# Kernel optimization log

Hardware: AMD Instinct MI355X
Metric: run time of the kernel (lower is better)

Reference implementation:

```python
import jax, jax.numpy as jnp
import numpy as np

C = 256
GROUPS = 32
EPS = 1e-6


def setup_inputs() -> dict:
    key = jax.random.key(0)
    ks = jax.random.split(key, 11)
    b, c, h, w, d = 4, C, 16, 16, 16
    s = 0.02
    return {
        "x": jax.random.normal(ks[0], (b, c, h, w, d), jnp.float32),
        "gn_w": jnp.ones((c,), jnp.float32),
        "gn_b": jnp.zeros((c,), jnp.float32),
        "wq": jax.random.normal(ks[1], (c, c), jnp.float32) * s,
        "bq": jnp.zeros((c,), jnp.float32),
        "wk": jax.random.normal(ks[2], (c, c), jnp.float32) * s,
        "bk": jnp.zeros((c,), jnp.float32),
        "wv": jax.random.normal(ks[3], (c, c), jnp.float32) * s,
        "bv": jnp.zeros((c,), jnp.float32),
        "wo": jax.random.normal(ks[4], (c, c), jnp.float32) * s,
        "bo": jnp.zeros((c,), jnp.float32),
    }


def group_norm(x, w, b):
    bsz, c, h, wd, d = x.shape
    xg = x.reshape(bsz, GROUPS, c // GROUPS, h, wd, d)
    mean = xg.mean(axis=(2, 3, 4, 5), keepdims=True)
    var = xg.var(axis=(2, 3, 4, 5), keepdims=True)
    xg = (xg - mean) * jax.lax.rsqrt(var + EPS)
    x = xg.reshape(bsz, c, h, wd, d)
    return x * w[None, :, None, None, None] + b[None, :, None, None, None]


def conv1(x, w, b):
    # 1x1x1 conv == channel-mixing matmul; x: [b,c,h,w,d], w: [out,in]
    return jnp.einsum('oc,bchwd->bohwd', w, x) + b[None, :, None, None, None]


def reference(x, gn_w, gn_b, wq, bq, wk, bk, wv, bv, wo, bo):
    b, c, h, w, d = x.shape
    scale = c ** (-0.5)
    xn = group_norm(x, gn_w, gn_b)
    q = conv1(xn, wq, bq).reshape(b, c, h * w * d)
    k = conv1(xn, wk, bk).reshape(b, c, h * w * d)
    v = conv1(xn, wv, bv).reshape(b, c, h * w * d)
    attn = jnp.einsum('bci,bcj->bij', q, k) * scale  # [b, N, N]
    attn = jax.nn.softmax(attn, axis=2)
    out = jnp.einsum('bij,bcj->bci', attn, v).reshape(b, c, h, w, d)
    out = conv1(out, wo, bo)
    return x + out
```

## Files before the change

kernel.cpp:

```cpp
#include <hip/hip_runtime.h>
#include <hip/hip_bf16.h>

#define BB 4
#define CC 256
#define NN 4096
#define BBNN (BB * NN)
#define NGROUPS 32
#define CPG 8
#define EPSG 1e-6f
#define QKSCL 0.30028063f
#define KSPLIT 4
#define JITERS (NN / KSPLIT / 64)
#define KSTRIDE 272

typedef __bf16 bf16x8 __attribute__((ext_vector_type(8)));
typedef float  f32x4  __attribute__((ext_vector_type(4)));

typedef __attribute__((address_space(1))) const void g_void;
typedef __attribute__((address_space(3))) void l_void;

__device__ __forceinline__ unsigned short f2bf(float f) {
  unsigned u = __builtin_bit_cast(unsigned, f);
  u += 0x7fffu + ((u >> 16) & 1u);
  return (unsigned short)(u >> 16);
}
__device__ __forceinline__ float bf2f(unsigned short s) {
  return __builtin_bit_cast(float, (unsigned)s << 16);
}

__device__ __forceinline__ f32x4 mfma16(bf16x8 a, bf16x8 b, f32x4 c) {
  return __builtin_amdgcn_mfma_f32_16x16x32_bf16(a, b, c, 0, 0, 0);
}
__device__ __forceinline__ f32x4 mfma8(long a, long b, f32x4 c) {
  return __builtin_amdgcn_mfma_f32_16x16x32_fp8_fp8(a, b, c, 0, 0, 0);
}

__device__ __forceinline__ bf16x8 ldfrag(const unsigned short* p) {
  return __builtin_bit_cast(bf16x8, *(const uint4*)p);
}

__global__ __launch_bounds__(256) void pre(const float* __restrict__ wq,
    const float* __restrict__ wk, const float* __restrict__ wv,
    const float* __restrict__ wo, const float* __restrict__ x,
    unsigned short* __restrict__ wbf, float* __restrict__ part) {
  if (blockIdx.x < 256) {
    int mat = blockIdx.x >> 6, blk = blockIdx.x & 63;
    const float* s = mat == 0 ? wq : mat == 1 ? wk : mat == 2 ? wv : wo;
    int i = (blk * 256 + threadIdx.x) * 4;
    float4 v = *(const float4*)&s[i];
    unsigned short* d = wbf + (size_t)mat * CC * CC + i;
    d[0] = f2bf(v.x); d[1] = f2bf(v.y); d[2] = f2bf(v.z); d[3] = f2bf(v.w);
    return;
  }
  int bx = blockIdx.x - 256;
  int pair = bx >> 1, h = bx & 1;
  const float* xp = x + (size_t)pair * (CPG * NN) + (size_t)h * (CPG * NN / 2);
  float s = 0.f, s2 = 0.f;
  for (int i = threadIdx.x; i < CPG * NN / 8; i += 256) {
    float4 v = ((const float4*)xp)[i];
    s += v.x + v.y + v.z + v.w;
    s2 += v.x * v.x + v.y * v.y + v.z * v.z + v.w * v.w;
  }
  for (int o = 32; o; o >>= 1) { s += __shfl_down(s, o); s2 += __shfl_down(s2, o); }
  __shared__ float rs[4], rs2[4];
  int wid = threadIdx.x >> 6, lane = threadIdx.x & 63;
  if (lane == 0) { rs[wid] = s; rs2[wid] = s2; }
  __syncthreads();
  if (threadIdx.x == 0) {
    part[bx * 2 + 0] = rs[0] + rs[1] + rs[2] + rs[3];
    part[bx * 2 + 1] = rs2[0] + rs2[1] + rs2[2] + rs2[3];
  }
}

__global__ __launch_bounds__(256) void gqkv(const float* __restrict__ x,
    const float* __restrict__ gw, const float* __restrict__ gb,
    const float* __restrict__ part, const unsigned short* __restrict__ wbf,
    const float* __restrict__ bq, const float* __restrict__ bk,
    const float* __restrict__ bv,
    unsigned char* __restrict__ q8, unsigned char* __restrict__ k8,
    unsigned char* __restrict__ v8) {
  const int low = blockIdx.x & 7;
  const int b = low & 3, shalf = low >> 2;
  const int t = blockIdx.x >> 3;
  const int mode = t >> 5;
  const int u = t & 31;
  const int sidx = (u >> 4) * 2 + shalf;
  const int nt = sidx * 16 + (u & 15);
  const int n0 = nt * 64;
  __shared__ unsigned short Xs[64][CC + 8];
  int tid = threadIdx.x;
  const float* xb = x + (size_t)b * CC * NN;
#pragma unroll
  for (int tt = 0; tt < 2; ++tt) {
    int item = tt * 256 + tid;
    int g = item >> 4, nc = item & 15;
    int pair = b * NGROUPS + g;
    float s = part[pair * 4 + 0] + part[pair * 4 + 2];
    float s2 = part[pair * 4 + 1] + part[pair * 4 + 3];
    float mean = s / (CPG * NN);
    float inv = rsqrtf(s2 / (CPG * NN) - mean * mean + EPSG);
    unsigned short row[4][8];
#pragma unroll
    for (int cc = 0; cc < 8; ++cc) {
      int c = g * 8 + cc;
      float wv = gw[c];
      float scv = inv * wv;
      float biv = gb[c] - mean * scv;
      float4 v = *(const float4*)&xb[(size_t)c * NN + n0 + nc * 4];
      row[0][cc] = f2bf(v.x * scv + biv);
      row[1][cc] = f2bf(v.y * scv + biv);
      row[2][cc] = f2bf(v.z * scv + biv);
      row[3][cc] = f2bf(v.w * scv + biv);
    }
#pragma unroll
    for (int r = 0; r < 4; ++r)
      *(uint4*)&Xs[nc * 4 + r][g * 8] = *(const uint4*)&row[r][0];
  }
  __syncthreads();
  int w = tid >> 6, lane = tid & 63;
  int m = lane & 15, q4 = lane >> 4;
  if (mode < 2) {
    bf16x8 xa[8];
#pragma unroll
    for (int k = 0; k < 8; ++k)
      xa[k] = ldfrag(&Xs[w * 16 + m][k * 32 + q4 * 8]);
    const unsigned short* W = wbf + (size_t)mode * CC * CC;
    const float* bias = mode ? bk : bq;
    unsigned char* dst = mode ? k8 : q8;
    for (int ot = 0; ot < 16; ++ot) {
      f32x4 acc = {0.f, 0.f, 0.f, 0.f};
#pragma unroll
      for (int k = 0; k < 8; ++k) {
        bf16x8 bf = ldfrag(&W[(size_t)(ot * 16 + m) * CC + k * 32 + q4 * 8]);
        acc = mfma16(xa[k], bf, acc);
      }
      int o = ot * 16 + m;
      float bia = bias[o];
      unsigned pk01 = __builtin_amdgcn_cvt_pk_fp8_f32(
          (acc[0] + bia) * QKSCL, (acc[1] + bia) * QKSCL, 0u, false);
      unsigned pk23 = __builtin_amdgcn_cvt_pk_fp8_f32(
          (acc[2] + bia) * QKSCL, (acc[3] + bia) * QKSCL, 0u, false);
      size_t base = ((size_t)b * NN + n0 + w * 16 + q4 * 4) * CC + o;
      dst[base]          = (unsigned char)(pk01 & 0xff);
      dst[base + CC]     = (unsigned char)((pk01 >> 8) & 0xff);
      dst[base + 2 * CC] = (unsigned char)(pk23 & 0xff);
      dst[base + 3 * CC] = (unsigned char)((pk23 >> 8) & 0xff);
    }
  } else {
    const unsigned short* Wv = wbf + 2 * CC * CC;
    for (int ot = 0; ot < 4; ++ot) {
      int o0 = w * 64 + ot * 16;
      bf16x8 af[8];
#pragma unroll
      for (int k = 0; k < 8; ++k)
        af[k] = ldfrag(&Wv[(size_t)(o0 + m) * CC + k * 32 + q4 * 8]);
#pragma unroll
      for (int nt4 = 0; nt4 < 4; ++nt4) {
        f32x4 acc = {0.f, 0.f, 0.f, 0.f};
#pragma unroll
        for (int k = 0; k < 8; ++k) {
          bf16x8 bfr = ldfrag(&Xs[nt4 * 16 + m][k * 32 + q4 * 8]);
          acc = mfma16(af[k], bfr, acc);
        }
        int j = nt4 * 16 + m;
        int jp = (j & 0x23) | ((j & 0x0C) << 1) | ((j & 0x10) >> 2);
        int n = n0 + jp;
        int o = o0 + q4 * 4;
        unsigned pk01 = __builtin_amdgcn_cvt_pk_fp8_f32(acc[0] + bv[o], acc[1] + bv[o + 1], 0u, false);
        unsigned pk23 = __builtin_amdgcn_cvt_pk_fp8_f32(acc[2] + bv[o + 2], acc[3] + bv[o + 3], 0u, false);
        size_t base = ((size_t)b * CC + o) * NN + n;
        v8[base]          = (unsigned char)(pk01 & 0xff);
        v8[base + NN]     = (unsigned char)((pk01 >> 8) & 0xff);
        v8[base + 2 * NN] = (unsigned char)(pk23 & 0xff);
        v8[base + 3 * NN] = (unsigned char)((pk23 >> 8) & 0xff);
      }
    }
  }
}

__device__ __forceinline__ void stageK8(const unsigned char* __restrict__ kp,
    int j0, unsigned char* Kb, int tid) {
#pragma unroll
  for (int t = 0; t < 2; ++t) {
    int item = t * 512 + tid;
    int row = item / 17, g = item % 17;
    int gs = (g == 16) ? 0 : g;
    const unsigned char* gp = kp + (size_t)(j0 + row) * CC + gs * 16;
    __builtin_amdgcn_global_load_lds((g_void*)gp, (l_void*)(Kb + item * 16), 16, 0, 0);
  }
  if (tid < 64) {
    int item = 1024 + tid;
    int row = item / 17, g = item % 17;
    int gs = (g == 16) ? 0 : g;
    const unsigned char* gp = kp + (size_t)(j0 + row) * CC + gs * 16;
    __builtin_amdgcn_global_load_lds((g_void*)gp, (l_void*)(Kb + item * 16), 16, 0, 0);
  }
}
__device__ __forceinline__ void stageV8(const unsigned char* __restrict__ vp,
    int j0, unsigned char* Vb, int tid) {
#pragma unroll
  for (int t = 0; t < 2; ++t) {
    int item = t * 512 + tid;
    int row = item >> 2, gl = item & 3;
    int gg = gl ^ (row & 3);
    const unsigned char* g = vp + (size_t)row * NN + j0 + gg * 16;
    __builtin_amdgcn_global_load_lds((g_void*)g, (l_void*)(Vb + item * 16), 16, 0, 0);
  }
}

__global__ __launch_bounds__(512, 4) void attn(const unsigned char* __restrict__ q8,
    const unsigned char* __restrict__ k8, const unsigned char* __restrict__ v8,
    unsigned short* __restrict__ accP, float* __restrict__ mlP) {
  const int grp = blockIdx.x & 15;
  const int s = grp >> 2, b = grp & 3;
  const int it = blockIdx.x >> 4;
  const int i0 = it * 128;
  __shared__ __align__(16) unsigned char pool[67584];
  unsigned char* Kd0 = pool;
  unsigned char* Kd1 = pool + 17408;
  unsigned char* Vd0 = pool + 34816;
  unsigned char* Vd1 = pool + 51200;
  int tid = threadIdx.x, w = tid >> 6, lane = tid & 63;
  int m = lane & 15, q4 = lane >> 4;
  int q4h = q4 >> 1, q4l = q4 & 1;
  const unsigned char* kp = k8 + (size_t)b * NN * CC;
  const unsigned char* vp = v8 + (size_t)b * CC * NN;
  long qa[8];
#pragma unroll
  for (int kc = 0; kc < 8; ++kc)
    qa[kc] = *(const long*)&q8[((size_t)b * NN + i0 + w * 16 + m) * CC + kc * 32 + q4 * 8];
  f32x4 acc[16];
#pragma unroll
  for (int i = 0; i < 16; ++i) acc[i] = (f32x4){0.f, 0.f, 0.f, 0.f};
  float mrow = -1e30f, lrow = 0.f;
  const int jbase = s * (NN / KSPLIT);
  stageK8(kp, jbase, Kd0, tid);
  stageV8(vp, jbase, Vd0, tid);
  const unsigned char* Kbase0 = Kd0 + m * KSTRIDE + q4 * 8;
  const unsigned char* Kbase1 = Kd1 + m * KSTRIDE + q4 * 8;
  for (int jt = 0; jt < JITERS; ++jt) {
    __syncthreads();
    const unsigned char* Kbase = (jt & 1) ? Kbase1 : Kbase0;
    const unsigned char* Vs    = (jt & 1) ? Vd1 : Vd0;
    if (jt + 1 < JITERS) {
      stageK8(kp, jbase + (jt + 1) * 64, (jt & 1) ? Kd0 : Kd1, tid);
      stageV8(vp, jbase + (jt + 1) * 64, (jt & 1) ? Vd0 : Vd1, tid);
    }
    f32x4 sv[4];
    __builtin_amdgcn_s_setprio(1);
#pragma unroll
    for (int jt4 = 0; jt4 < 4; ++jt4) {
      f32x4 a = {0.f, 0.f, 0.f, 0.f};
#pragma unroll
      for (int kc = 0; kc < 8; ++kc) {
        long kf = *(const long*)&Kbase[jt4 * 16 * KSTRIDE + kc * 32];
        a = mfma8(kf, qa[kc], a);
      }
      sv[jt4] = a;
    }
    __builtin_amdgcn_s_setprio(0);
    float mx = fmaxf(fmaxf(fmaxf(sv[0][0], sv[0][1]), fmaxf(sv[0][2], sv[0][3])),
                     fmaxf(fmaxf(sv[1][0], sv[1][1]), fmaxf(sv[1][2], sv[1][3])));
    mx = fmaxf(mx, fmaxf(fmaxf(fmaxf(sv[2][0], sv[2][1]), fmaxf(sv[2][2], sv[2][3])),
                         fmaxf(fmaxf(sv[3][0], sv[3][1]), fmaxf(sv[3][2], sv[3][3]))));
    mx = fmaxf(mx, __shfl_xor(mx, 16));
    mx = fmaxf(mx, __shfl_xor(mx, 32));
    float mnew = fmaxf(mrow, mx);
    float alpha = exp2f(mrow - mnew);
    mrow = mnew;
    float rsum = 0.f;
    unsigned pd[4];
#pragma unroll
    for (int jt4 = 0; jt4 < 4; ++jt4) {
      float e0 = exp2f(sv[jt4][0] - mnew);
      float e1 = exp2f(sv[jt4][1] - mnew);
      float e2 = exp2f(sv[jt4][2] - mnew);
      float e3 = exp2f(sv[jt4][3] - mnew);
      rsum += (e0 + e1) + (e2 + e3);
      unsigned d = __builtin_amdgcn_cvt_pk_fp8_f32(e0, e1, 0u, false);
      pd[jt4] = __builtin_amdgcn_cvt_pk_fp8_f32(e2, e3, d, true);
    }
    rsum += __shfl_xor(rsum, 16);
    rsum += __shfl_xor(rsum, 32);
    lrow = lrow * alpha + rsum;
    if (__any(alpha != 1.0f)) {
#pragma unroll
      for (int ct = 0; ct < 16; ++ct) acc[ct] *= alpha;
    }
    int voff = ((q4h) ^ (m & 3)) * 16 + q4l * 8;
    int voff1 = ((2 + q4h) ^ (m & 3)) * 16 + q4l * 8;
    __builtin_amdgcn_s_setprio(1);
#pragma unroll
    for (int p = 0; p < 2; ++p) {
      uint2 pu = {pd[2 * p], pd[2 * p + 1]};
      long pT = __builtin_bit_cast(long, pu);
      int vo = p ? voff1 : voff;
#pragma unroll
      for (int ct = 0; ct < 16; ++ct) {
        long vf = *(const long*)&Vs[(ct * 16 + m) * 64 + vo];
        acc[ct] = mfma8(vf, pT, acc[ct]);
      }
    }
    __builtin_amdgcn_s_setprio(0);
  }
  size_t rq = (size_t)(s * BB + b) * NN + i0 + w * 16 + m;
  if (q4 == 0) {
    mlP[rq * 2 + 0] = mrow;
    mlP[rq * 2 + 1] = lrow;
  }
  __syncthreads();
  unsigned short* tp = (unsigned short*)pool;
  int wh = w >> 2, wl = w & 3;
#pragma unroll
  for (int half = 0; half < 2; ++half) {
    if (wh == half) {
#pragma unroll
      for (int ct = 0; ct < 16; ++ct) {
        unsigned lo = f2bf(acc[ct][0]) | ((unsigned)f2bf(acc[ct][1]) << 16);
        unsigned hi = f2bf(acc[ct][2]) | ((unsigned)f2bf(acc[ct][3]) << 16);
        uint2 pk = {lo, hi};
        *(uint2*)&tp[(wl * 16 + m) * 260 + ct * 16 + q4 * 4] = pk;
      }
    }
    __syncthreads();
#pragma unroll
    for (int u = 0; u < 4; ++u) {
      int id = u * 512 + tid;
      int row = id >> 5, ck = id & 31;
      uint4 v = *(const uint4*)&tp[row * 260 + ck * 8];
      *(uint4*)&accP[((size_t)(s * BB + b) * NN + i0 + half * 64 + row) * CC + ck * 8] = v;
    }
    __syncthreads();
  }
}

__global__ __launch_bounds__(256) void proj(const unsigned short* __restrict__ accP,
    const float* __restrict__ mlP, const unsigned short* __restrict__ Wo,
    const float* __restrict__ bo, const float* __restrict__ x,
    float* __restrict__ out) {
  const int b = blockIdx.x >> 7, nt = blockIdx.x & 127;
  const int n0 = nt * 32;
  __shared__ unsigned short As[32][CC + 8];
  __shared__ float wr[KSPLIT][36];
  int tid = threadIdx.x;
  if (tid < 32) {
    int n = n0 + tid;
    float mv[KSPLIT], lv[KSPLIT], M = -1e30f;
#pragma unroll
    for (int s = 0; s < KSPLIT; ++s) {
      size_t rq = (size_t)(s * BB + b) * NN + n;
      mv[s] = mlP[rq * 2];
      lv[s] = mlP[rq * 2 + 1];
      M = fmaxf(M, mv[s]);
    }
    float ws[KSPLIT], d = 0.f;
#pragma unroll
    for (int s = 0; s < KSPLIT; ++s) {
      ws[s] = exp2f(mv[s] - M);
      d += lv[s] * ws[s];
    }
    float inv = 1.f / d;
#pragma unroll
    for (int s = 0; s < KSPLIT; ++s) wr[s][tid] = ws[s] * inv;
  }
  __syncthreads();
#pragma unroll
  for (int i = 0; i < 4; ++i) {
    int id = tid + 256 * i;
    int r = id >> 5, ck = id & 31;
    int n = n0 + r;
    float f[8] = {0.f, 0.f, 0.f, 0.f, 0.f, 0.f, 0.f, 0.f};
#pragma unroll
    for (int s = 0; s < KSPLIT; ++s) {
      uint4 a = *(const uint4*)&accP[((size_t)(s * BB + b) * NN + n) * CC + ck * 8];
      const unsigned* p = (const unsigned*)&a;
      float wgt = wr[s][r];
#pragma unroll
      for (int k = 0; k < 4; ++k) {
        f[k * 2 + 0] += bf2f((unsigned short)(p[k] & 0xffff)) * wgt;
        f[k * 2 + 1] += bf2f((unsigned short)(p[k] >> 16)) * wgt;
      }
    }
    unsigned short ov[8];
#pragma unroll
    for (int k = 0; k < 8; ++k) ov[k] = f2bf(f[k]);
    *(uint4*)&As[r][ck * 8] = *(const uint4*)&ov[0];
  }
  __syncthreads();
  int w = tid >> 6, lane = tid & 63, m = lane & 15, q4 = lane >> 4;
  for (int ot = 0; ot < 4; ++ot) {
    int o0 = w * 64 + ot * 16;
    bf16x8 af[8];
#pragma unroll
    for (int k = 0; k < 8; ++k)
      af[k] = ldfrag(&Wo[(size_t)(o0 + m) * CC + k * 32 + q4 * 8]);
#pragma unroll
    for (int nt4 = 0; nt4 < 2; ++nt4) {
      f32x4 a = {0.f, 0.f, 0.f, 0.f};
#pragma unroll
      for (int k = 0; k < 8; ++k) {
        bf16x8 bf = ldfrag(&As[nt4 * 16 + m][k * 32 + q4 * 8]);
        a = mfma16(af[k], bf, a);
      }
      int n = n0 + nt4 * 16 + m;
#pragma unroll
      for (int r = 0; r < 4; ++r) {
        int o = o0 + q4 * 4 + r;
        size_t idx = ((size_t)b * CC + o) * NN + n;
        out[idx] = x[idx] + bo[o] + a[r];
      }
    }
  }
}

extern "C" void kernel_launch(void* const* d_in, const int* in_sizes, int n_in,
                              void* d_out, int out_size, void* d_ws, size_t ws_size,
                              hipStream_t stream) {
  const float* x  = (const float*)d_in[0];
  const float* gw = (const float*)d_in[1];
  const float* gb = (const float*)d_in[2];
  const float* wq = (const float*)d_in[3];
  const float* bq = (const float*)d_in[4];
  const float* wk = (const float*)d_in[5];
  const float* bk = (const float*)d_in[6];
  const float* wv = (const float*)d_in[7];
  const float* bv = (const float*)d_in[8];
  const float* wo = (const float*)d_in[9];
  const float* bo = (const float*)d_in[10];

  const size_t M4 = (size_t)BB * NN * CC;
  unsigned short* wbf = (unsigned short*)d_ws;
  unsigned short* accPb = wbf + 4 * CC * CC;
  float* mlP  = (float*)(accPb + (size_t)KSPLIT * M4);
  float* part = mlP + (size_t)KSPLIT * BBNN * 2;
  unsigned char* q8 = (unsigned char*)(part + 512);
  unsigned char* k8 = q8 + M4;
  unsigned char* v8 = k8 + M4;

  pre<<<512, 256, 0, stream>>>(wq, wk, wv, wo, x, wbf, part);
  gqkv<<<768, 256, 0, stream>>>(x, gw, gb, part, wbf, bq, bk, bv, q8, k8, v8);
  attn<<<KSPLIT * BB * 32, 512, 0, stream>>>(q8, k8, v8, accPb, mlP);
  proj<<<512, 256, 0, stream>>>(accPb, mlP, wbf + 3 * CC * CC, bo, x, (float*)d_out);
}
```

Measured before the change: 249.2 us.

## Process two 16-row query tiles per wave in attention, halve block size

Each wave of the attention kernel now handles 32 query rows (two 16-row tiles) instead of 16, and the block shrinks from 512 to 256 threads with launch bounds (256,2). Every K and V fragment read from LDS now feeds two MFMAs, which halves LDS traffic per MFMA. The cost is doubled accumulator and Q register state (two sets of 16 f32x4 accumulators) and fewer resident waves, so there is less latency hiding and possible register pressure or spilling.

New measurement: 224.5 us. 9.9% less time.

```diff
diff --git a/kernel.cpp b/kernel.cpp
--- a/kernel.cpp
+++ b/kernel.cpp
@@ -181,8 +181,8 @@
 __device__ __forceinline__ void stageK8(const unsigned char* __restrict__ kp,
     int j0, unsigned char* Kb, int tid) {
 #pragma unroll
-  for (int t = 0; t < 2; ++t) {
-    int item = t * 512 + tid;
+  for (int t = 0; t < 4; ++t) {
+    int item = t * 256 + tid;
     int row = item / 17, g = item % 17;
     int gs = (g == 16) ? 0 : g;
     const unsigned char* gp = kp + (size_t)(j0 + row) * CC + gs * 16;
@@ -199,8 +199,8 @@
 __device__ __forceinline__ void stageV8(const unsigned char* __restrict__ vp,
     int j0, unsigned char* Vb, int tid) {
 #pragma unroll
-  for (int t = 0; t < 2; ++t) {
-    int item = t * 512 + tid;
+  for (int t = 0; t < 4; ++t) {
+    int item = t * 256 + tid;
     int row = item >> 2, gl = item & 3;
     int gg = gl ^ (row & 3);
     const unsigned char* g = vp + (size_t)row * NN + j0 + gg * 16;
@@ -208,7 +208,7 @@
   }
 }
 
-__global__ __launch_bounds__(512, 4) void attn(const unsigned char* __restrict__ q8,
+__global__ __launch_bounds__(256, 2) void attn(const unsigned char* __restrict__ q8,
     const unsigned char* __restrict__ k8, const unsigned char* __restrict__ v8,
     unsigned short* __restrict__ accP, float* __restrict__ mlP) {
   const int grp = blockIdx.x & 15;
@@ -225,14 +225,20 @@
   int q4h = q4 >> 1, q4l = q4 & 1;
   const unsigned char* kp = k8 + (size_t)b * NN * CC;
   const unsigned char* vp = v8 + (size_t)b * CC * NN;
-  long qa[8];
-#pragma unroll
-  for (int kc = 0; kc < 8; ++kc)
-    qa[kc] = *(const long*)&q8[((size_t)b * NN + i0 + w * 16 + m) * CC + kc * 32 + q4 * 8];
-  f32x4 acc[16];
-#pragma unroll
-  for (int i = 0; i < 16; ++i) acc[i] = (f32x4){0.f, 0.f, 0.f, 0.f};
-  float mrow = -1e30f, lrow = 0.f;
+  const int iA0 = i0 + w * 32;
+  long qaA[8], qaB[8];
+#pragma unroll
+  for (int kc = 0; kc < 8; ++kc) {
+    qaA[kc] = *(const long*)&q8[((size_t)b * NN + iA0 + m) * CC + kc * 32 + q4 * 8];
+    qaB[kc] = *(const long*)&q8[((size_t)b * NN + iA0 + 16 + m) * CC + kc * 32 + q4 * 8];
+  }
+  f32x4 accA[16], accB[16];
+#pragma unroll
+  for (int i = 0; i < 16; ++i) {
+    accA[i] = (f32x4){0.f, 0.f, 0.f, 0.f};
+    accB[i] = (f32x4){0.f, 0.f, 0.f, 0.f};
+  }
+  float mrowA = -1e30f, lrowA = 0.f, mrowB = -1e30f, lrowB = 0.f;
   const int jbase = s * (NN / KSPLIT);
   stageK8(kp, jbase, Kd0, tid);
   stageV8(vp, jbase, Vd0, tid);
@@ -246,86 +252,119 @@
       stageK8(kp, jbase + (jt + 1) * 64, (jt & 1) ? Kd0 : Kd1, tid);
       stageV8(vp, jbase + (jt + 1) * 64, (jt & 1) ? Vd0 : Vd1, tid);
     }
-    f32x4 sv[4];
+    f32x4 svA[4], svB[4];
     __builtin_amdgcn_s_setprio(1);
 #pragma unroll
     for (int jt4 = 0; jt4 < 4; ++jt4) {
-      f32x4 a = {0.f, 0.f, 0.f, 0.f};
+      f32x4 aA = {0.f, 0.f, 0.f, 0.f};
+      f32x4 aB = {0.f, 0.f, 0.f, 0.f};
 #pragma unroll
       for (int kc = 0; kc < 8; ++kc) {
         long kf = *(const long*)&Kbase[jt4 * 16 * KSTRIDE + kc * 32];
-        a = mfma8(kf, qa[kc], a);
-      }
-      sv[jt4] = a;
+        aA = mfma8(kf, qaA[kc], aA);
+        aB = mfma8(kf, qaB[kc], aB);
+      }
+      svA[jt4] = aA;
+      svB[jt4] = aB;
     }
     __builtin_amdgcn_s_setprio(0);
-    float mx = fmaxf(fmaxf(fmaxf(sv[0][0], sv[0][1]), fmaxf(sv[0][2], sv[0][3])),
-                     fmaxf(fmaxf(sv[1][0], sv[1][1]), fmaxf(sv[1][2], sv[1][3])));
-    mx = fmaxf(mx, fmaxf(fmaxf(fmaxf(sv[2][0], sv[2][1]), fmaxf(sv[2][2], sv[2][3])),
-                         fmaxf(fmaxf(sv[3][0], sv[3][1]), fmaxf(sv[3][2], sv[3][3]))));
-    mx = fmaxf(mx, __shfl_xor(mx, 16));
-    mx = fmaxf(mx, __shfl_xor(mx, 32));
-    float mnew = fmaxf(mrow, mx);
-    float alpha = exp2f(mrow - mnew);
-    mrow = mnew;
-    float rsum = 0.f;
-    unsigned pd[4];
+    float mxA = -1e30f, mxB = -1e30f;
 #pragma unroll
     for (int jt4 = 0; jt4 < 4; ++jt4) {
-      float e0 = exp2f(sv[jt4][0] - mnew);
-      float e1 = exp2f(sv[jt4][1] - mnew);
-      float e2 = exp2f(sv[jt4][2] - mnew);
-      float e3 = exp2f(sv[jt4][3] - mnew);
-      rsum += (e0 + e1) + (e2 + e3);
+      mxA = fmaxf(mxA, fmaxf(fmaxf(svA[jt4][0], svA[jt4][1]), fmaxf(svA[jt4][2], svA[jt4][3])));
+      mxB = fmaxf(mxB, fmaxf(fmaxf(svB[jt4][0], svB[jt4][1]), fmaxf(svB[jt4][2], svB[jt4][3])));
+    }
+    mxA = fmaxf(mxA, __shfl_xor(mxA, 16));
+    mxA = fmaxf(mxA, __shfl_xor(mxA, 32));
+    mxB = fmaxf(mxB, __shfl_xor(mxB, 16));
+    mxB = fmaxf(mxB, __shfl_xor(mxB, 32));
+    float mnewA = fmaxf(mrowA, mxA);
+    float mnewB = fmaxf(mrowB, mxB);
+    float alphaA = exp2f(mrowA - mnewA);
+    float alphaB = exp2f(mrowB - mnewB);
+    mrowA = mnewA;
+    mrowB = mnewB;
+    float rsumA = 0.f, rsumB = 0.f;
+    unsigned pdA[4], pdB[4];
+#pragma unroll
+    for (int jt4 = 0; jt4 < 4; ++jt4) {
+      float e0 = exp2f(svA[jt4][0] - mnewA);
+      float e1 = exp2f(svA[jt4][1] - mnewA);
+      float e2 = exp2f(svA[jt4][2] - mnewA);
+      float e3 = exp2f(svA[jt4][3] - mnewA);
+      rsumA += (e0 + e1) + (e2 + e3);
       unsigned d = __builtin_amdgcn_cvt_pk_fp8_f32(e0, e1, 0u, false);
-      pd[jt4] = __builtin_amdgcn_cvt_pk_fp8_f32(e2, e3, d, true);
-    }
-    rsum += __shfl_xor(rsum, 16);
-    rsum += __shfl_xor(rsum, 32);
-    lrow = lrow * alpha + rsum;
-    if (__any(alpha != 1.0f)) {
-#pragma unroll
-      for (int ct = 0; ct < 16; ++ct) acc[ct] *= alpha;
+      pdA[jt4] = __builtin_amdgcn_cvt_pk_fp8_f32(e2, e3, d, true);
+      float f0 = exp2f(svB[jt4][0] - mnewB);
+      float f1 = exp2f(svB[jt4][1] - mnewB);
+      float f2 = exp2f(svB[jt4][2] - mnewB);
+      float f3 = exp2f(svB[jt4][3] - mnewB);
+      rsumB += (f0 + f1) + (f2 + f3);
+      unsigned e = __builtin_amdgcn_cvt_pk_fp8_f32(f0, f1, 0u, false);
+      pdB[jt4] = __builtin_amdgcn_cvt_pk_fp8_f32(f2, f3, e, true);
+    }
+    rsumA += __shfl_xor(rsumA, 16);
+    rsumA += __shfl_xor(rsumA, 32);
+    rsumB += __shfl_xor(rsumB, 16);
+    rsumB += __shfl_xor(rsumB, 32);
+    lrowA = lrowA * alphaA + rsumA;
+    lrowB = lrowB * alphaB + rsumB;
+    if (__any(alphaA != 1.0f)) {
+#pragma unroll
+      for (int ct = 0; ct < 16; ++ct) accA[ct] *= alphaA;
+    }
+    if (__any(alphaB != 1.0f)) {
+#pragma unroll
+      for (int ct = 0; ct < 16; ++ct) accB[ct] *= alphaB;
     }
     int voff = ((q4h) ^ (m & 3)) * 16 + q4l * 8;
     int voff1 = ((2 + q4h) ^ (m & 3)) * 16 + q4l * 8;
     __builtin_amdgcn_s_setprio(1);
 #pragma unroll
     for (int p = 0; p < 2; ++p) {
-      uint2 pu = {pd[2 * p], pd[2 * p + 1]};
-      long pT = __builtin_bit_cast(long, pu);
+      uint2 puA = {pdA[2 * p], pdA[2 * p + 1]};
+      uint2 puB = {pdB[2 * p], pdB[2 * p + 1]};
+      long pTA = __builtin_bit_cast(long, puA);
+      long pTB = __builtin_bit_cast(long, puB);
       int vo = p ? voff1 : voff;
 #pragma unroll
       for (int ct = 0; ct < 16; ++ct) {
         long vf = *(const long*)&Vs[(ct * 16 + m) * 64 + vo];
-        acc[ct] = mfma8(vf, pT, acc[ct]);
+        accA[ct] = mfma8(vf, pTA, accA[ct]);
+        accB[ct] = mfma8(vf, pTB, accB[ct]);
       }
     }
     __builtin_amdgcn_s_setprio(0);
   }
-  size_t rq = (size_t)(s * BB + b) * NN + i0 + w * 16 + m;
+  size_t rqA = (size_t)(s * BB + b) * NN + iA0 + m;
   if (q4 == 0) {
-    mlP[rq * 2 + 0] = mrow;
-    mlP[rq * 2 + 1] = lrow;
+    mlP[rqA * 2 + 0] = mrowA;
+    mlP[rqA * 2 + 1] = lrowA;
+    mlP[(rqA + 16) * 2 + 0] = mrowB;
+    mlP[(rqA + 16) * 2 + 1] = lrowB;
   }
   __syncthreads();
   unsigned short* tp = (unsigned short*)pool;
-  int wh = w >> 2, wl = w & 3;
 #pragma unroll
   for (int half = 0; half < 2; ++half) {
-    if (wh == half) {
+    if ((w >> 1) == half) {
+      int rbase = (w & 1) * 32;
 #pragma unroll
       for (int ct = 0; ct < 16; ++ct) {
-        unsigned lo = f2bf(acc[ct][0]) | ((unsigned)f2bf(acc[ct][1]) << 16);
-        unsigned hi = f2bf(acc[ct][2]) | ((unsigned)f2bf(acc[ct][3]) << 16);
-        uint2 pk = {lo, hi};
-        *(uint2*)&tp[(wl * 16 + m) * 260 + ct * 16 + q4 * 4] = pk;
+        unsigned loA = f2bf(accA[ct][0]) | ((unsigned)f2bf(accA[ct][1]) << 16);
+        unsigned hiA = f2bf(accA[ct][2]) | ((unsigned)f2bf(accA[ct][3]) << 16);
+        uint2 pkA = {loA, hiA};
+        *(uint2*)&tp[(rbase + m) * 260 + ct * 16 + q4 * 4] = pkA;
+        unsigned loB = f2bf(accB[ct][0]) | ((unsigned)f2bf(accB[ct][1]) << 16);
+        unsigned hiB = f2bf(accB[ct][2]) | ((unsigned)f2bf(accB[ct][3]) << 16);
+        uint2 pkB = {loB, hiB};
+        *(uint2*)&tp[(rbase + 16 + m) * 260 + ct * 16 + q4 * 4] = pkB;
       }
     }
     __syncthreads();
 #pragma unroll
-    for (int u = 0; u < 4; ++u) {
-      int id = u * 512 + tid;
+    for (int u = 0; u < 8; ++u) {
+      int id = u * 256 + tid;
       int row = id >> 5, ck = id & 31;
       uint4 v = *(const uint4*)&tp[row * 260 + ck * 8];
       *(uint4*)&accP[((size_t)(s * BB + b) * NN + i0 + half * 64 + row) * CC + ck * 8] = v;
@@ -439,6 +478,6 @@
 
   pre<<<512, 256, 0, stream>>>(wq, wk, wv, wo, x, wbf, part);
   gqkv<<<768, 256, 0, stream>>>(x, gw, gb, part, wbf, bq, bk, bv, q8, k8, v8);
-  attn<<<KSPLIT * BB * 32, 512, 0, stream>>>(q8, k8, v8, accPb, mlP);
+  attn<<<KSPLIT * BB * 32, 256, 0, stream>>>(q8, k8, v8, accPb, mlP);
   proj<<<512, 256, 0, stream>>>(accPb, mlP, wbf + 3 * CC * CC, bo, x, (float*)d_out);
 }
```
